# Kernel tuning notes

Hardware: AMD Instinct MI355X
Metric: run time of the kernel (lower is better)

Reference implementation:

```python
import jax, jax.numpy as jnp
import numpy as np


def setup_inputs() -> dict:
    key = jax.random.key(0)
    k1, k2 = jax.random.split(key)
    x = jax.random.normal(k1, (8, 8192, 128), dtype=jnp.float32)
    embed = jax.random.normal(k2, (1024, 128), dtype=jnp.float32)
    return {"x": x, "embed": embed}


def reference(x, embed):
    """EuclideanCodebook.forward, eval mode, c=0 (Euclidean path).

    x:     [..., D] inputs
    embed: [K, D] codebook
    Returns (quantize [..., D], embed_ind [...]).
    """
    shape = x.shape
    xf = x.reshape(-1, shape[-1])                      # (N, D)
    x2 = jnp.sum(xf * xf, axis=1, keepdims=True)       # (N, 1)
    e2 = jnp.sum(embed * embed, axis=1)                # (K,)
    dist = -(x2 - 2.0 * (xf @ embed.T) + e2[None, :])  # (N, K)
    embed_ind = jnp.argmax(dist, axis=-1)              # (N,)
    embed_ind = embed_ind.reshape(shape[:-1])          # postprocess_emb
    quantize = embed[embed_ind]                        # dequantize (gather)
    return quantize, embed_ind
```

## Files before the change

kernel.cpp:

```cpp
#include <hip/hip_runtime.h>

typedef _Float16 half8 __attribute__((ext_vector_type(8)));
typedef float f32x4 __attribute__((ext_vector_type(4)));

#define DD 128


__global__ void prep_frags_kernel(const float* __restrict__ embed,
                                  char* __restrict__ frag, int total) {
  int t = blockIdx.x * blockDim.x + threadIdx.x;
  if (t >= total) return;
  int lane = t & 63;
  int idx = (t >> 6) & 7;
  int c = t >> 9;
  int s = idx >> 1;
  int hl = idx & 1;
  int n = c * 16 + (lane & 15);
  int kb = s * 32 + ((lane >> 4) << 3);
  const float* src = embed + (size_t)n * DD + kb;
  _Float16* dst = (_Float16*)(frag + (size_t)c * 8192 + idx * 1024 + lane * 16);
#pragma unroll
  for (int j = 0; j < 8; ++j) {
    float v = src[j];
    _Float16 hi = (_Float16)v;
    dst[j] = hl ? (_Float16)(v - (float)hi) : hi;
  }
}

__global__ void prep_e2_kernel(const float* __restrict__ embed,
                               float* __restrict__ e2neg, int total) {
  int t = blockIdx.x * blockDim.x + threadIdx.x;
  if (t >= total) return;
  int lane = t & 63;
  int c = t >> 6;
  int n = c * 16 + (lane & 15);
  const float* src = embed + (size_t)n * DD;
  double s = 0.0;
  for (int j = 0; j < DD; ++j) { double v = (double)src[j]; s += v * v; }
  e2neg[c * 64 + lane] = (float)(-s);
}

__global__ __launch_bounds__(256) void vq_argmin_kernel(
    const float* __restrict__ x, const float* __restrict__ embed,
    const char* __restrict__ wsf, const float* __restrict__ wse,
    float* __restrict__ out_q, float* __restrict__ out_i, int nch) {
  const int lane = threadIdx.x & 63;
  const int w = threadIdx.x >> 6;
  const int m16 = lane & 15;
  const int g = lane >> 4;
  const int row0 = blockIdx.x * 128 + w * 32;

  half8 ah[2][4], al[2][4];
#pragma unroll
  for (int t = 0; t < 2; ++t) {
    const float* xrow = x + (size_t)(row0 + t * 16 + m16) * DD;
#pragma unroll
    for (int s = 0; s < 4; ++s) {
      const float* p = xrow + s * 32 + g * 8;
      f32x4 v0 = *(const f32x4*)(p);
      f32x4 v1 = *(const f32x4*)(p + 4);
#pragma unroll
      for (int j = 0; j < 4; ++j) {
        float v = v0[j];
        _Float16 hi = (_Float16)v;
        ah[t][s][j] = hi;
        al[t][s][j] = (_Float16)(v - (float)hi);
      }
#pragma unroll
      for (int j = 0; j < 4; ++j) {
        float v = v1[j];
        _Float16 hi = (_Float16)v;
        ah[t][s][4 + j] = hi;
        al[t][s][4 + j] = (_Float16)(v - (float)hi);
      }
    }
  }

  float bestv0[4], bestv1[4];
  int besti0[4], besti1[4];
#pragma unroll
  for (int r = 0; r < 4; ++r) {
    bestv0[r] = -__builtin_inff();
    bestv1[r] = -__builtin_inff();
    besti0[r] = 0;
    besti1[r] = 0;
  }

  half8 bhA[4], blA[4], bhB[4], blB[4];
  float neA, neB;

#define LOADB(BH, BL, NE, C)                                        \
  do {                                                              \
    const char* pf = wsf + (size_t)(C)*8192 + lane * 16;            \
    const char* pf1 = pf + 4096;                                    \
    BH[0] = *(const half8*)(pf);                                    \
    BL[0] = *(const half8*)(pf + 1024);                             \
    BH[1] = *(const half8*)(pf + 2048);                             \
    BL[1] = *(const half8*)(pf + 3072);                             \
    BH[2] = *(const half8*)(pf1);                                   \
    BL[2] = *(const half8*)(pf1 + 1024);                            \
    BH[3] = *(const half8*)(pf1 + 2048);                            \
    BL[3] = *(const half8*)(pf1 + 3072);                            \
    NE = wse[(size_t)(C)*64 + lane];                                \
  } while (0)

#define COMPUTE(BH, BL, NE, C)                                               \
  do {                                                                       \
    f32x4 acc0 = {0.f, 0.f, 0.f, 0.f};                                       \
    f32x4 acc1 = {0.f, 0.f, 0.f, 0.f};                                       \
    _Pragma("unroll") for (int s = 0; s < 4; ++s) {                          \
      acc0 = __builtin_amdgcn_mfma_f32_16x16x32_f16(ah[0][s], BH[s], acc0,   \
                                                    0, 0, 0);                \
      acc1 = __builtin_amdgcn_mfma_f32_16x16x32_f16(ah[1][s], BH[s], acc1,   \
                                                    0, 0, 0);                \
      acc0 = __builtin_amdgcn_mfma_f32_16x16x32_f16(al[0][s], BH[s], acc0,   \
                                                    0, 0, 0);                \
      acc1 = __builtin_amdgcn_mfma_f32_16x16x32_f16(al[1][s], BH[s], acc1,   \
                                                    0, 0, 0);                \
      acc0 = __builtin_amdgcn_mfma_f32_16x16x32_f16(ah[0][s], BL[s], acc0,   \
                                                    0, 0, 0);                \
      acc1 = __builtin_amdgcn_mfma_f32_16x16x32_f16(ah[1][s], BL[s], acc1,   \
                                                    0, 0, 0);                \
    }                                                                        \
    const int n_ = (C)*16 + m16;                                             \
    _Pragma("unroll") for (int r = 0; r < 4; ++r) {                          \
      float s0 = fmaf(2.f, acc0[r], NE);                                     \
      if (s0 > bestv0[r]) { bestv0[r] = s0; besti0[r] = n_; }                \
      float s1 = fmaf(2.f, acc1[r], NE);                                     \
      if (s1 > bestv1[r]) { bestv1[r] = s1; besti1[r] = n_; }                \
    }                                                                        \
  } while (0)

  LOADB(bhA, blA, neA, 0);
  for (int c = 0; c < nch; c += 2) {
    LOADB(bhB, blB, neB, c + 1);
    COMPUTE(bhA, blA, neA, c);
    if (c + 2 < nch) LOADB(bhA, blA, neA, c + 2);
    COMPUTE(bhB, blB, neB, c + 1);
  }
#undef LOADB
#undef COMPUTE

#pragma unroll
  for (int off = 1; off < 16; off <<= 1) {
#pragma unroll
    for (int r = 0; r < 4; ++r) {
      float ov0 = __shfl_xor(bestv0[r], off, 64);
      int oi0 = __shfl_xor(besti0[r], off, 64);
      if (ov0 > bestv0[r] || (ov0 == bestv0[r] && oi0 < besti0[r])) {
        bestv0[r] = ov0;
        besti0[r] = oi0;
      }
      float ov1 = __shfl_xor(bestv1[r], off, 64);
      int oi1 = __shfl_xor(besti1[r], off, 64);
      if (ov1 > bestv1[r] || (ov1 == bestv1[r] && oi1 < besti1[r])) {
        bestv1[r] = ov1;
        besti1[r] = oi1;
      }
    }
  }

#pragma unroll
  for (int t = 0; t < 2; ++t) {
#pragma unroll
    for (int r = 0; r < 4; ++r) {
      const int row = row0 + t * 16 + g * 4 + r;
      const int idx = t ? besti1[r] : besti0[r];
      if (m16 == 0) out_i[row] = (float)idx;
      const f32x4* src = (const f32x4*)(embed + (size_t)idx * DD) + m16 * 2;
      f32x4* dst = (f32x4*)(out_q + (size_t)row * DD) + m16 * 2;
      dst[0] = src[0];
      dst[1] = src[1];
    }
  }
}

__global__ void vq_fallback_kernel(const float* __restrict__ x,
                                   const float* __restrict__ embed,
                                   float* __restrict__ out_q,
                                   float* __restrict__ out_i, int N, int K) {
  int row = blockIdx.x * blockDim.x + threadIdx.x;
  if (row >= N) return;
  const float* xr = x + (size_t)row * DD;
  float xv[DD];
  for (int j = 0; j < DD; ++j) xv[j] = xr[j];
  double best = -1e300;
  int bi = 0;
  for (int k = 0; k < K; ++k) {
    const float* e = embed + (size_t)k * DD;
    double acc = 0.0;
    for (int j = 0; j < DD; ++j) {
      double d = (double)xv[j] - (double)e[j];
      acc += d * d;
    }
    double sc = -acc;
    if (sc > best) { best = sc; bi = k; }
  }
  out_i[row] = (float)bi;
  for (int j = 0; j < DD; ++j)
    out_q[(size_t)row * DD + j] = embed[(size_t)bi * DD + j];
}

extern "C" void kernel_launch(void* const* d_in, const int* in_sizes, int n_in,
                              void* d_out, int out_size, void* d_ws,
                              size_t ws_size, hipStream_t stream) {
  const float* x = (const float*)d_in[0];
  const float* embed = (const float*)d_in[1];
  const int N = in_sizes[0] / DD;
  const int K = in_sizes[1] / DD;
  float* out_q = (float*)d_out;
  float* out_i = out_q + (size_t)N * DD;

  const int nch = K / 16;
  const size_t frag_bytes = (size_t)nch * 8192;
  const size_t e2_bytes = (size_t)nch * 256;
  const size_t need = frag_bytes + e2_bytes;

  if (ws_size < need || (N % 128) != 0 || (K % 16) != 0) {
    vq_fallback_kernel<<<(N + 255) / 256, 256, 0, stream>>>(x, embed, out_q,
                                                            out_i, N, K);
    return;
  }

  char* wsf = (char*)d_ws;
  float* wse = (float*)(wsf + frag_bytes);

  const int total_f = nch * 8 * 64;
  prep_frags_kernel<<<(total_f + 255) / 256, 256, 0, stream>>>(embed, wsf,
                                                               total_f);
  const int total_e = nch * 64;
  prep_e2_kernel<<<(total_e + 255) / 256, 256, 0, stream>>>(embed, wse,
                                                            total_e);
  vq_argmin_kernel<<<N / 128, 256, 0, stream>>>(x, embed, wsf, wse, out_q,
                                                out_i, nch);
}
```

Measured before the change: 70.37 us.

## Triple-buffer codebook fragment loads and split MFMA accumulator chains

The codebook fragment prefetch grows from two register buffers to three, so each chunk's loads are issued two compute steps before use. Each chunk now keeps four independent accumulators (high and low parts for each of the two row tiles) instead of two, which shortens the dependent MFMA chains. The aim is to hide global load latency and MFMA dependency stalls, at the cost of more VGPRs and possibly lower occupancy. Tail chunks are handled after the loop, and fewer than three chunks now go to the fallback kernel.

```diff
diff --git a/kernel.cpp b/kernel.cpp
--- a/kernel.cpp
+++ b/kernel.cpp
@@ -86,58 +86,74 @@
     besti1[r] = 0;
   }
 
-  half8 bhA[4], blA[4], bhB[4], blB[4];
-  float neA, neB;
-
-#define LOADB(BH, BL, NE, C)                                        \
-  do {                                                              \
-    const char* pf = wsf + (size_t)(C)*8192 + lane * 16;            \
-    const char* pf1 = pf + 4096;                                    \
-    BH[0] = *(const half8*)(pf);                                    \
-    BL[0] = *(const half8*)(pf + 1024);                             \
-    BH[1] = *(const half8*)(pf + 2048);                             \
-    BL[1] = *(const half8*)(pf + 3072);                             \
-    BH[2] = *(const half8*)(pf1);                                   \
-    BL[2] = *(const half8*)(pf1 + 1024);                            \
-    BH[3] = *(const half8*)(pf1 + 2048);                            \
-    BL[3] = *(const half8*)(pf1 + 3072);                            \
-    NE = wse[(size_t)(C)*64 + lane];                                \
+  half8 bh[3][4], bl[3][4];
+
+#define LOADB(I, C)                                              \
+  do {                                                           \
+    const char* pf_ = wsf + (size_t)(C)*8192 + lane * 16;        \
+    bh[I][0] = *(const half8*)(pf_);                             \
+    bl[I][0] = *(const half8*)(pf_ + 1024);                      \
+    bh[I][1] = *(const half8*)(pf_ + 2048);                      \
+    bl[I][1] = *(const half8*)(pf_ + 3072);                      \
+    bh[I][2] = *(const half8*)(pf_ + 4096);                      \
+    bl[I][2] = *(const half8*)(pf_ + 5120);                      \
+    bh[I][3] = *(const half8*)(pf_ + 6144);                      \
+    bl[I][3] = *(const half8*)(pf_ + 7168);                      \
   } while (0)
 
-#define COMPUTE(BH, BL, NE, C)                                               \
-  do {                                                                       \
-    f32x4 acc0 = {0.f, 0.f, 0.f, 0.f};                                       \
-    f32x4 acc1 = {0.f, 0.f, 0.f, 0.f};                                       \
-    _Pragma("unroll") for (int s = 0; s < 4; ++s) {                          \
-      acc0 = __builtin_amdgcn_mfma_f32_16x16x32_f16(ah[0][s], BH[s], acc0,   \
-                                                    0, 0, 0);                \
-      acc1 = __builtin_amdgcn_mfma_f32_16x16x32_f16(ah[1][s], BH[s], acc1,   \
-                                                    0, 0, 0);                \
-      acc0 = __builtin_amdgcn_mfma_f32_16x16x32_f16(al[0][s], BH[s], acc0,   \
-                                                    0, 0, 0);                \
-      acc1 = __builtin_amdgcn_mfma_f32_16x16x32_f16(al[1][s], BH[s], acc1,   \
-                                                    0, 0, 0);                \
-      acc0 = __builtin_amdgcn_mfma_f32_16x16x32_f16(ah[0][s], BL[s], acc0,   \
-                                                    0, 0, 0);                \
-      acc1 = __builtin_amdgcn_mfma_f32_16x16x32_f16(ah[1][s], BL[s], acc1,   \
-                                                    0, 0, 0);                \
-    }                                                                        \
-    const int n_ = (C)*16 + m16;                                             \
-    _Pragma("unroll") for (int r = 0; r < 4; ++r) {                          \
-      float s0 = fmaf(2.f, acc0[r], NE);                                     \
-      if (s0 > bestv0[r]) { bestv0[r] = s0; besti0[r] = n_; }                \
-      float s1 = fmaf(2.f, acc1[r], NE);                                     \
-      if (s1 > bestv1[r]) { bestv1[r] = s1; besti1[r] = n_; }                \
-    }                                                                        \
+#define COMPUTE(I, C)                                                          \
+  do {                                                                         \
+    const float ne_ = wse[(size_t)(C)*64 + lane];                              \
+    f32x4 aH0 = {0.f, 0.f, 0.f, 0.f};                                          \
+    f32x4 aH1 = {0.f, 0.f, 0.f, 0.f};                                          \
+    f32x4 aL0 = {0.f, 0.f, 0.f, 0.f};                                          \
+    f32x4 aL1 = {0.f, 0.f, 0.f, 0.f};                                          \
+    _Pragma("unroll") for (int s = 0; s < 4; ++s) {                            \
+      aH0 = __builtin_amdgcn_mfma_f32_16x16x32_f16(ah[0][s], bh[I][s], aH0,    \
+                                                   0, 0, 0);                   \
+      aH1 = __builtin_amdgcn_mfma_f32_16x16x32_f16(ah[1][s], bh[I][s], aH1,    \
+                                                   0, 0, 0);                   \
+      aL0 = __builtin_amdgcn_mfma_f32_16x16x32_f16(al[0][s], bh[I][s], aL0,    \
+                                                   0, 0, 0);                   \
+      aL1 = __builtin_amdgcn_mfma_f32_16x16x32_f16(al[1][s], bh[I][s], aL1,    \
+                                                   0, 0, 0);                   \
+      aL0 = __builtin_amdgcn_mfma_f32_16x16x32_f16(ah[0][s], bl[I][s], aL0,    \
+                                                   0, 0, 0);                   \
+      aL1 = __builtin_amdgcn_mfma_f32_16x16x32_f16(ah[1][s], bl[I][s], aL1,    \
+                                                   0, 0, 0);                   \
+    }                                                                          \
+    const int n_ = (C)*16 + m16;                                               \
+    _Pragma("unroll") for (int r = 0; r < 4; ++r) {                            \
+      float s0 = fmaf(2.f, aH0[r] + aL0[r], ne_);                              \
+      if (s0 > bestv0[r]) { bestv0[r] = s0; besti0[r] = n_; }                  \
+      float s1 = fmaf(2.f, aH1[r] + aL1[r], ne_);                              \
+      if (s1 > bestv1[r]) { bestv1[r] = s1; besti1[r] = n_; }                  \
+    }                                                                          \
   } while (0)
 
-  LOADB(bhA, blA, neA, 0);
-  for (int c = 0; c < nch; c += 2) {
-    LOADB(bhB, blB, neB, c + 1);
-    COMPUTE(bhA, blA, neA, c);
-    if (c + 2 < nch) LOADB(bhA, blA, neA, c + 2);
-    COMPUTE(bhB, blB, neB, c + 1);
-  }
+  LOADB(0, 0);
+  LOADB(1, 1);
+  LOADB(2, 2);
+  int c = 0;
+  for (; c + 2 < nch; c += 3) {
+    COMPUTE(0, c);
+    {
+      const int cc = (c + 3 < nch) ? c + 3 : 0;
+      LOADB(0, cc);
+    }
+    COMPUTE(1, c + 1);
+    {
+      const int cc = (c + 4 < nch) ? c + 4 : 0;
+      LOADB(1, cc);
+    }
+    COMPUTE(2, c + 2);
+    {
+      const int cc = (c + 5 < nch) ? c + 5 : 0;
+      LOADB(2, cc);
+    }
+  }
+  if (c < nch) COMPUTE(0, c);
+  if (c + 1 < nch) COMPUTE(1, c + 1);
 #undef LOADB
 #undef COMPUTE
 
@@ -216,7 +232,7 @@
   const size_t e2_bytes = (size_t)nch * 256;
   const size_t need = frag_bytes + e2_bytes;
 
-  if (ws_size < need || (N % 128) != 0 || (K % 16) != 0) {
+  if (ws_size < need || (N % 128) != 0 || (K % 16) != 0 || nch < 3) {
     vq_fallback_kernel<<<(N + 255) / 256, 256, 0, stream>>>(x, embed, out_q,
                                                             out_i, N, K);
     return;
```

After: 73.18 us. 4.0% more time.

## Split codebook across wave pairs and merge argmin via shared memory

Applied to the files above, without the earlier changes.

Each block now covers 64 rows instead of 128, and its four waves are split into two pairs that each scan half of the codebook chunks for the same 32 rows. The partial best values and indices from the second pair are exchanged through shared memory and merged before the cross-lane reduction and output. This doubles the grid size to improve occupancy and latency hiding across CUs. The cost is that each x row's split-fp16 fragments are loaded and converted twice, plus an extra shared-memory merge and a block barrier.

```diff
diff --git a/kernel.cpp b/kernel.cpp
--- a/kernel.cpp
+++ b/kernel.cpp
@@ -48,7 +48,12 @@
   const int w = threadIdx.x >> 6;
   const int m16 = lane & 15;
   const int g = lane >> 4;
-  const int row0 = blockIdx.x * 128 + w * 32;
+  const int row0 = blockIdx.x * 64 + (w & 1) * 32;
+  const int kh = w >> 1;
+  const int nc2 = nch >> 1;
+
+  __shared__ float vbuf[2][64][8];
+  __shared__ int ibuf[2][64][8];
 
   half8 ah[2][4], al[2][4];
 #pragma unroll
@@ -131,15 +136,45 @@
     }                                                                        \
   } while (0)
 
-  LOADB(bhA, blA, neA, 0);
-  for (int c = 0; c < nch; c += 2) {
+  const int c0 = kh * nc2;
+  const int cE = c0 + nc2;
+  LOADB(bhA, blA, neA, c0);
+  for (int c = c0; c < cE; c += 2) {
     LOADB(bhB, blB, neB, c + 1);
     COMPUTE(bhA, blA, neA, c);
-    if (c + 2 < nch) LOADB(bhA, blA, neA, c + 2);
+    if (c + 2 < cE) LOADB(bhA, blA, neA, c + 2);
     COMPUTE(bhB, blB, neB, c + 1);
   }
 #undef LOADB
 #undef COMPUTE
+
+  if (w >= 2) {
+#pragma unroll
+    for (int r = 0; r < 4; ++r) {
+      vbuf[w - 2][lane][r] = bestv0[r];
+      vbuf[w - 2][lane][4 + r] = bestv1[r];
+      ibuf[w - 2][lane][r] = besti0[r];
+      ibuf[w - 2][lane][4 + r] = besti1[r];
+    }
+  }
+  __syncthreads();
+  if (w >= 2) return;
+
+#pragma unroll
+  for (int r = 0; r < 4; ++r) {
+    float pv0 = vbuf[w][lane][r];
+    int pi0 = ibuf[w][lane][r];
+    if (pv0 > bestv0[r] || (pv0 == bestv0[r] && pi0 < besti0[r])) {
+      bestv0[r] = pv0;
+      besti0[r] = pi0;
+    }
+    float pv1 = vbuf[w][lane][4 + r];
+    int pi1 = ibuf[w][lane][4 + r];
+    if (pv1 > bestv1[r] || (pv1 == bestv1[r] && pi1 < besti1[r])) {
+      bestv1[r] = pv1;
+      besti1[r] = pi1;
+    }
+  }
 
 #pragma unroll
   for (int off = 1; off < 16; off <<= 1) {
@@ -216,7 +251,7 @@
   const size_t e2_bytes = (size_t)nch * 256;
   const size_t need = frag_bytes + e2_bytes;
 
-  if (ws_size < need || (N % 128) != 0 || (K % 16) != 0) {
+  if (ws_size < need || (N % 64) != 0 || (K % 16) != 0 || (nch % 4) != 0) {
     vq_fallback_kernel<<<(N + 255) / 256, 256, 0, stream>>>(x, embed, out_q,
                                                             out_i, N, K);
     return;
@@ -231,6 +266,6 @@
   const int total_e = nch * 64;
   prep_e2_kernel<<<(total_e + 255) / 256, 256, 0, stream>>>(embed, wse,
                                                             total_e);
-  vq_argmin_kernel<<<N / 128, 256, 0, stream>>>(x, embed, wsf, wse, out_q,
-                                                out_i, nch);
-}
+  vq_argmin_kernel<<<N / 64, 256, 0, stream>>>(x, embed, wsf, wse, out_q,
+                                               out_i, nch);
+}
```

Result: slower. 76.17 us (+8.2%).

## Stage codebook fragments cooperatively in LDS and merge prep kernels

Applied to the files above, without the earlier changes.

In the main kernel, each wave used to load every codebook fragment chunk straight from global memory. Now the four waves each load a quarter of the chunk into a double-buffered LDS tile and read it back from there, with a block barrier per chunk. This cuts redundant global and L2 traffic by four times, at the cost of a __syncthreads every iteration and 16 KB of LDS. The two prep kernels are also merged into one launch, where the idx==0 threads compute the squared norms.

```diff
diff --git a/kernel.cpp b/kernel.cpp
--- a/kernel.cpp
+++ b/kernel.cpp
@@ -2,12 +2,14 @@
 
 typedef _Float16 half8 __attribute__((ext_vector_type(8)));
 typedef float f32x4 __attribute__((ext_vector_type(4)));
+typedef unsigned int u32x4 __attribute__((ext_vector_type(4)));
 
 #define DD 128
 
 
-__global__ void prep_frags_kernel(const float* __restrict__ embed,
-                                  char* __restrict__ frag, int total) {
+__global__ void prep_kernel(const float* __restrict__ embed,
+                            char* __restrict__ frag,
+                            float* __restrict__ e2neg, int total) {
   int t = blockIdx.x * blockDim.x + threadIdx.x;
   if (t >= total) return;
   int lane = t & 63;
@@ -25,19 +27,12 @@
     _Float16 hi = (_Float16)v;
     dst[j] = hl ? (_Float16)(v - (float)hi) : hi;
   }
-}
-
-__global__ void prep_e2_kernel(const float* __restrict__ embed,
-                               float* __restrict__ e2neg, int total) {
-  int t = blockIdx.x * blockDim.x + threadIdx.x;
-  if (t >= total) return;
-  int lane = t & 63;
-  int c = t >> 6;
-  int n = c * 16 + (lane & 15);
-  const float* src = embed + (size_t)n * DD;
-  double s = 0.0;
-  for (int j = 0; j < DD; ++j) { double v = (double)src[j]; s += v * v; }
-  e2neg[c * 64 + lane] = (float)(-s);
+  if (idx == 0) {
+    const float* e = embed + (size_t)n * DD;
+    double acc = 0.0;
+    for (int j = 0; j < DD; ++j) { double v = (double)e[j]; acc += v * v; }
+    e2neg[c * 64 + lane] = (float)(-acc);
+  }
 }
 
 __global__ __launch_bounds__(256) void vq_argmin_kernel(
@@ -50,6 +45,8 @@
   const int g = lane >> 4;
   const int row0 = blockIdx.x * 128 + w * 32;
 
+  __shared__ alignas(16) char lds[2][8192];
+
   half8 ah[2][4], al[2][4];
 #pragma unroll
   for (int t = 0; t < 2; ++t) {
@@ -86,60 +83,68 @@
     besti1[r] = 0;
   }
 
-  half8 bhA[4], blA[4], bhB[4], blB[4];
-  float neA, neB;
-
-#define LOADB(BH, BL, NE, C)                                        \
-  do {                                                              \
-    const char* pf = wsf + (size_t)(C)*8192 + lane * 16;            \
-    const char* pf1 = pf + 4096;                                    \
-    BH[0] = *(const half8*)(pf);                                    \
-    BL[0] = *(const half8*)(pf + 1024);                             \
-    BH[1] = *(const half8*)(pf + 2048);                             \
-    BL[1] = *(const half8*)(pf + 3072);                             \
-    BH[2] = *(const half8*)(pf1);                                   \
-    BL[2] = *(const half8*)(pf1 + 1024);                            \
-    BH[3] = *(const half8*)(pf1 + 2048);                            \
-    BL[3] = *(const half8*)(pf1 + 3072);                            \
-    NE = wse[(size_t)(C)*64 + lane];                                \
-  } while (0)
-
-#define COMPUTE(BH, BL, NE, C)                                               \
-  do {                                                                       \
-    f32x4 acc0 = {0.f, 0.f, 0.f, 0.f};                                       \
-    f32x4 acc1 = {0.f, 0.f, 0.f, 0.f};                                       \
-    _Pragma("unroll") for (int s = 0; s < 4; ++s) {                          \
-      acc0 = __builtin_amdgcn_mfma_f32_16x16x32_f16(ah[0][s], BH[s], acc0,   \
-                                                    0, 0, 0);                \
-      acc1 = __builtin_amdgcn_mfma_f32_16x16x32_f16(ah[1][s], BH[s], acc1,   \
-                                                    0, 0, 0);                \
-      acc0 = __builtin_amdgcn_mfma_f32_16x16x32_f16(al[0][s], BH[s], acc0,   \
-                                                    0, 0, 0);                \
-      acc1 = __builtin_amdgcn_mfma_f32_16x16x32_f16(al[1][s], BH[s], acc1,   \
-                                                    0, 0, 0);                \
-      acc0 = __builtin_amdgcn_mfma_f32_16x16x32_f16(ah[0][s], BL[s], acc0,   \
-                                                    0, 0, 0);                \
-      acc1 = __builtin_amdgcn_mfma_f32_16x16x32_f16(ah[1][s], BL[s], acc1,   \
-                                                    0, 0, 0);                \
-    }                                                                        \
-    const int n_ = (C)*16 + m16;                                             \
-    _Pragma("unroll") for (int r = 0; r < 4; ++r) {                          \
-      float s0 = fmaf(2.f, acc0[r], NE);                                     \
-      if (s0 > bestv0[r]) { bestv0[r] = s0; besti0[r] = n_; }                \
-      float s1 = fmaf(2.f, acc1[r], NE);                                     \
-      if (s1 > bestv1[r]) { bestv1[r] = s1; besti1[r] = n_; }                \
-    }                                                                        \
-  } while (0)
-
-  LOADB(bhA, blA, neA, 0);
-  for (int c = 0; c < nch; c += 2) {
-    LOADB(bhB, blB, neB, c + 1);
-    COMPUTE(bhA, blA, neA, c);
-    if (c + 2 < nch) LOADB(bhA, blA, neA, c + 2);
-    COMPUTE(bhB, blB, neB, c + 1);
-  }
-#undef LOADB
-#undef COMPUTE
+  {
+    const char* gs = wsf + (size_t)0 * 8192 + w * 2048 + lane * 16;
+    u32x4 s0 = *(const u32x4*)(gs);
+    u32x4 s1 = *(const u32x4*)(gs + 1024);
+    char* lw = &lds[0][w * 2048 + lane * 16];
+    *(u32x4*)(lw) = s0;
+    *(u32x4*)(lw + 1024) = s1;
+  }
+  __syncthreads();
+
+  for (int c = 0; c < nch; ++c) {
+    const int buf = c & 1;
+    u32x4 t0, t1;
+    const bool pre = (c + 1 < nch);
+    if (pre) {
+      const char* gs = wsf + (size_t)(c + 1) * 8192 + w * 2048 + lane * 16;
+      t0 = *(const u32x4*)(gs);
+      t1 = *(const u32x4*)(gs + 1024);
+    }
+    const float ne_ = wse[(size_t)c * 64 + lane];
+
+    const char* fb = &lds[buf][0];
+    half8 bh[4], bl[4];
+#pragma unroll
+    for (int s = 0; s < 4; ++s) {
+      bh[s] = *(const half8*)(fb + (2 * s) * 1024 + lane * 16);
+      bl[s] = *(const half8*)(fb + (2 * s + 1) * 1024 + lane * 16);
+    }
+
+    f32x4 acc0 = {0.f, 0.f, 0.f, 0.f};
+    f32x4 acc1 = {0.f, 0.f, 0.f, 0.f};
+#pragma unroll
+    for (int s = 0; s < 4; ++s) {
+      acc0 = __builtin_amdgcn_mfma_f32_16x16x32_f16(ah[0][s], bh[s], acc0, 0,
+                                                    0, 0);
+      acc1 = __builtin_amdgcn_mfma_f32_16x16x32_f16(ah[1][s], bh[s], acc1, 0,
+                                                    0, 0);
+      acc0 = __builtin_amdgcn_mfma_f32_16x16x32_f16(al[0][s], bh[s], acc0, 0,
+                                                    0, 0);
+      acc1 = __builtin_amdgcn_mfma_f32_16x16x32_f16(al[1][s], bh[s], acc1, 0,
+                                                    0, 0);
+      acc0 = __builtin_amdgcn_mfma_f32_16x16x32_f16(ah[0][s], bl[s], acc0, 0,
+                                                    0, 0);
+      acc1 = __builtin_amdgcn_mfma_f32_16x16x32_f16(ah[1][s], bl[s], acc1, 0,
+                                                    0, 0);
+    }
+    const int n_ = c * 16 + m16;
+#pragma unroll
+    for (int r = 0; r < 4; ++r) {
+      float s0 = fmaf(2.f, acc0[r], ne_);
+      if (s0 > bestv0[r]) { bestv0[r] = s0; besti0[r] = n_; }
+      float s1 = fmaf(2.f, acc1[r], ne_);
+      if (s1 > bestv1[r]) { bestv1[r] = s1; besti1[r] = n_; }
+    }
+
+    if (pre) {
+      char* lw = &lds[buf ^ 1][w * 2048 + lane * 16];
+      *(u32x4*)(lw) = t0;
+      *(u32x4*)(lw + 1024) = t1;
+    }
+    __syncthreads();
+  }
 
 #pragma unroll
   for (int off = 1; off < 16; off <<= 1) {
@@ -226,11 +231,8 @@
   float* wse = (float*)(wsf + frag_bytes);
 
   const int total_f = nch * 8 * 64;
-  prep_frags_kernel<<<(total_f + 255) / 256, 256, 0, stream>>>(embed, wsf,
-                                                               total_f);
-  const int total_e = nch * 64;
-  prep_e2_kernel<<<(total_e + 255) / 256, 256, 0, stream>>>(embed, wse,
-                                                            total_e);
+  prep_kernel<<<(total_f + 255) / 256, 256, 0, stream>>>(embed, wsf, wse,
+                                                         total_f);
   vq_argmin_kernel<<<N / 128, 256, 0, stream>>>(x, embed, wsf, wse, out_q,
                                                 out_i, nch);
 }
```

Result: faster. 65.20 us (-7.3%).
